# Kernel tuning notes

Hardware: AMD Instinct MI355X
Metric: run time of the kernel (lower is better)

Reference implementation:

```python
import jax, jax.numpy as jnp
import numpy as np

N = 256
IL_MMI = 0.02      # insertion loss MMI
IMB = 0.01         # imbalance MMI
IL_CR = 0.02       # insertion loss Crossing
CT = 0.01          # cross talk Crossing


def _mmi_matrix():
    # 2x2 MMI: sqrt(1-IL)*[[t, i r],[i r, t]] with t=sqrt((1+imb)/2), r=sqrt((1-imb)/2)
    a = np.sqrt(1.0 - IL_MMI)
    t = np.sqrt((1.0 + IMB) / 2.0)
    r = np.sqrt((1.0 - IMB) / 2.0)
    mmi2 = a * np.array([[t, 1j * r], [1j * r, t]], dtype=np.complex64)
    # block-diagonal over even pairs (0,1),(2,3),...
    return jnp.asarray(np.kron(np.eye(N // 2, dtype=np.complex64), mmi2))


def _crossing_matrix():
    # pairs start at odd index 1; rows 0 and N-1 pass through with amplitude sqrt(1-IL)*sqrt(1-CT)
    a = np.sqrt(1.0 - IL_CR)
    thru = a * np.sqrt(1.0 - CT)
    cr2 = a * np.array([[np.sqrt(CT), 1j * np.sqrt(1.0 - CT)],
                        [1j * np.sqrt(1.0 - CT), np.sqrt(CT)]], dtype=np.complex64)
    M = np.zeros((N, N), dtype=np.complex64)
    M[0, 0] = thru
    for i in range(1, N - 1, 2):
        M[i:i + 2, i:i + 2] = cr2
    if N % 2 == 0:
        M[-1, -1] = thru
    return jnp.asarray(M)


def setup_inputs() -> dict:
    key = jax.random.key(0)
    thetas = jax.random.uniform(key, (N // 2 + 2, N), dtype=jnp.float32) * (2.0 * np.pi)
    return {"thetas": thetas}


def reference(thetas):
    MMI = _mmi_matrix()
    CR = _crossing_matrix()
    phases = jnp.exp(1j * thetas)  # [N//2+2, N] complex64; diag phase-shift layers

    # arch = ht[0] @ I  (diagonal left-multiply == row scaling)
    arch0 = jnp.diag(phases[0])

    def body(arch, ph):
        # one mesh stage with trailing crossing (iterations i = 0 .. N//2-2)
        arch = MMI @ arch
        arch = ph[:, None] * arch      # ht[i+1] @ arch
        arch = MMI @ arch
        arch = CR @ arch
        return arch, None

    arch, _ = jax.lax.scan(body, arch0, phases[1:N // 2])

    # last loop iteration (i = N//2-1): no crossing
    arch = MMI @ arch
    arch = phases[N // 2][:, None] * arch
    arch = MMI @ arch
    # final phase layer ht[N//2+1]
    arch = phases[N // 2 + 1][:, None] * arch
    return arch
```

## Files before the change

kernel.cpp:

```cpp
#include <hip/hip_runtime.h>


constexpr int N = 256;

__global__ __launch_bounds__(64)
void neuropuls_chain_kernel(const float* __restrict__ thetas,
                            float2* __restrict__ Abuf,
                            float2* __restrict__ Bbuf)
{
    const int lane = threadIdx.x;
    const bool isB = blockIdx.x >= 256;
    const int col  = blockIdx.x & 255;

    const float AT = sqrtf(0.98f * 0.505f);
    const float AR = sqrtf(0.98f * 0.495f);
    const float BT = sqrtf(0.98f * 0.01f);
    const float BR = sqrtf(0.98f * 0.99f);

    float vr[4] = {0.f, 0.f, 0.f, 0.f};
    float vi[4] = {0.f, 0.f, 0.f, 0.f};

    {
        const int r0 = col - 4 * lane;
        if (0 <= r0 && r0 < 4) {
            if (isB) { vr[r0] = 1.f; vi[r0] = 0.f; }
            else {
                float s0, c0;
                __sincosf(thetas[col], &s0, &c0);
                vr[r0] = c0; vi[r0] = s0;
            }
        }
    }

    const int s0     = isB ? 65 : 1;
    const int nCross = isB ? 63 : 64;

    const float* tp = thetas + s0 * N + 4 * lane;

    auto mmi_pair = [&](int x, int y) {
        float xr = vr[x], xi = vi[x], yr = vr[y], yi = vi[y];
        vr[x] = AT * xr - AR * yi;  vi[x] = AT * xi + AR * yr;
        vr[y] = AT * yr - AR * xi;  vi[y] = AT * yi + AR * xr;
    };
    auto phase4c = [&](const float sn[4], const float cs[4]) {
        #pragma unroll
        for (int j = 0; j < 4; ++j) {
            float r = vr[j], i = vi[j];
            vr[j] = cs[j] * r - sn[j] * i;
            vi[j] = cs[j] * i + sn[j] * r;
        }
    };
    auto crossing = [&]() {
        float pv3r = __shfl_up(vr[3], 1);
        float pv3i = __shfl_up(vi[3], 1);
        float nv0r = __shfl_down(vr[0], 1);
        float nv0i = __shfl_down(vi[0], 1);
        {
            float xr = vr[1], xi = vi[1], yr = vr[2], yi = vi[2];
            vr[1] = BT * xr - BR * yi;  vi[1] = BT * xi + BR * yr;
            vr[2] = BT * yr - BR * xi;  vi[2] = BT * yi + BR * xr;
        }
        {
            float yr = vr[0], yi = vi[0];
            float nr = BT * yr - BR * pv3i;
            float ni = BT * yi + BR * pv3r;
            vr[0] = (lane == 0) ? BR * yr : nr;
            vi[0] = (lane == 0) ? BR * yi : ni;
        }
        {
            float xr = vr[3], xi = vi[3];
            float nr = BT * xr - BR * nv0i;
            float ni = BT * xi + BR * nv0r;
            vr[3] = (lane == 63) ? BR * xr : nr;
            vi[3] = (lane == 63) ? BR * xi : ni;
        }
    };
    auto sincos4 = [](float4 th, float sn[4], float cs[4]) {
        __sincosf(th.x, &sn[0], &cs[0]);
        __sincosf(th.y, &sn[1], &cs[1]);
        __sincosf(th.z, &sn[2], &cs[2]);
        __sincosf(th.w, &sn[3], &cs[3]);
    };

    float snA[4], csA[4];
    float4 thN;
    {
        float4 t1 = *(const float4*)tp;  tp += N;
        thN = *(const float4*)tp;        tp += N;
        sincos4(t1, snA, csA);
    }

    #pragma unroll 2
    for (int it = 0; it < nCross - 1; ++it) {
        float4 thNN = *(const float4*)tp;  tp += N;
        float snB[4], csB[4];
        sincos4(thN, snB, csB);
        mmi_pair(0, 1); mmi_pair(2, 3);
        phase4c(snA, csA);
        mmi_pair(0, 1); mmi_pair(2, 3);
        crossing();
        #pragma unroll
        for (int j = 0; j < 4; ++j) { snA[j] = snB[j]; csA[j] = csB[j]; }
        thN = thNN;
    }

    mmi_pair(0, 1); mmi_pair(2, 3);
    phase4c(snA, csA);
    mmi_pair(0, 1); mmi_pair(2, 3);
    crossing();

    if (isB) {
        float sn[4], cs[4];
        sincos4(thN, sn, cs);
        mmi_pair(0, 1); mmi_pair(2, 3);
        phase4c(sn, cs);
        mmi_pair(0, 1); mmi_pair(2, 3);
        float4 thF = *(const float4*)(thetas + 129 * N + 4 * lane);
        sincos4(thF, sn, cs);
        phase4c(sn, cs);
    }

    float2* dst = (isB ? Bbuf : Abuf) + col * N + 4 * lane;
    #pragma unroll
    for (int j = 0; j < 4; ++j) dst[j] = make_float2(vr[j], vi[j]);
}

__global__ __launch_bounds__(256)
void neuropuls_combine_kernel(const float2* __restrict__ Abuf,
                              const float2* __restrict__ Bbuf,
                              float* __restrict__ out)
{
    __shared__ float2 Acol[N];
    const int c = blockIdx.x;
    const int r = threadIdx.x;

    Acol[r] = Abuf[c * N + r];
    __syncthreads();

    float accr = 0.f, acci = 0.f;
    #pragma unroll 8
    for (int k = 0; k < N; ++k) {
        float2 b = Bbuf[k * N + r];
        float2 a = Acol[k];
        accr += b.x * a.x - b.y * a.y;
        acci += b.x * a.y + b.y * a.x;
    }

    out[r * N + c]         = accr;
    out[N * N + r * N + c] = acci;
}

extern "C" void kernel_launch(void* const* d_in, const int* in_sizes, int n_in,
                              void* d_out, int out_size, void* d_ws, size_t ws_size,
                              hipStream_t stream)
{
    const float* thetas = (const float*)d_in[0];
    float2* Abuf = (float2*)d_ws;
    float2* Bbuf = Abuf + N * N;
    float* out = (float*)d_out;
    (void)in_sizes; (void)n_in; (void)out_size; (void)ws_size;

    neuropuls_chain_kernel<<<dim3(512), dim3(64), 0, stream>>>(thetas, Abuf, Bbuf);
    neuropuls_combine_kernel<<<dim3(256), dim3(256), 0, stream>>>(Abuf, Bbuf, out);
}
```

Measured before the change: 85.43 us.

## Fuse MMI-phase-MMI into one 2x2 complex matrix and tile the combine GEMM

The chain kernel now folds the MMI, phase and MMI sequence into one precomputed 2x2 complex matrix per pair, built from sincos values. This cuts the FMAs on the serial critical path in each stage. The combine kernel becomes a shared-memory tiled complex GEMM with 32x32 output tiles and 2x2 register blocking per thread, replacing the per-column reduction that streamed all of B from global memory. It launches 64 blocks instead of 256, so fewer CUs are busy, but each loaded value is reused more.

Measured after the change: 100.3 us. 17.4% more time.

```diff
diff --git a/kernel.cpp b/kernel.cpp
--- a/kernel.cpp
+++ b/kernel.cpp
@@ -12,10 +12,11 @@
     const bool isB = blockIdx.x >= 256;
     const int col  = blockIdx.x & 255;
 
-    const float AT = sqrtf(0.98f * 0.505f);
-    const float AR = sqrtf(0.98f * 0.495f);
-    const float BT = sqrtf(0.98f * 0.01f);
-    const float BR = sqrtf(0.98f * 0.99f);
+    const float BT  = sqrtf(0.98f * 0.01f);
+    const float BR  = sqrtf(0.98f * 0.99f);
+    const float AT2 = 0.98f * 0.505f;
+    const float AR2 = 0.98f * 0.495f;
+    const float ATR = 0.98f * sqrtf(0.505f * 0.495f);
 
     float vr[4] = {0.f, 0.f, 0.f, 0.f};
     float vi[4] = {0.f, 0.f, 0.f, 0.f};
@@ -23,7 +24,7 @@
     {
         const int r0 = col - 4 * lane;
         if (0 <= r0 && r0 < 4) {
-            if (isB) { vr[r0] = 1.f; vi[r0] = 0.f; }
+            if (isB) { vr[r0] = 1.f; }
             else {
                 float s0, c0;
                 __sincosf(thetas[col], &s0, &c0);
@@ -34,20 +35,36 @@
 
     const int s0     = isB ? 65 : 1;
     const int nCross = isB ? 63 : 64;
-
     const float* tp = thetas + s0 * N + 4 * lane;
 
-    auto mmi_pair = [&](int x, int y) {
-        float xr = vr[x], xi = vi[x], yr = vr[y], yi = vi[y];
-        vr[x] = AT * xr - AR * yi;  vi[x] = AT * xi + AR * yr;
-        vr[y] = AT * yr - AR * xi;  vi[y] = AT * yi + AR * xr;
+    float F[2][6], G[2][6];
+
+    auto buildF = [&](float4 th, float Fd[2][6]) {
+        float sn[4], cs[4];
+        __sincosf(th.x, &sn[0], &cs[0]);
+        __sincosf(th.y, &sn[1], &cs[1]);
+        __sincosf(th.z, &sn[2], &cs[2]);
+        __sincosf(th.w, &sn[3], &cs[3]);
+        #pragma unroll
+        for (int j = 0; j < 2; ++j) {
+            const int x = 2 * j, y = 2 * j + 1;
+            Fd[j][0] = AT2 * cs[x] - AR2 * cs[y];
+            Fd[j][1] = AT2 * sn[x] - AR2 * sn[y];
+            Fd[j][2] = -ATR * (sn[x] + sn[y]);
+            Fd[j][3] =  ATR * (cs[x] + cs[y]);
+            Fd[j][4] = AT2 * cs[y] - AR2 * cs[x];
+            Fd[j][5] = AT2 * sn[y] - AR2 * sn[x];
+        }
     };
-    auto phase4c = [&](const float sn[4], const float cs[4]) {
-        #pragma unroll
-        for (int j = 0; j < 4; ++j) {
-            float r = vr[j], i = vi[j];
-            vr[j] = cs[j] * r - sn[j] * i;
-            vi[j] = cs[j] * i + sn[j] * r;
+    auto applyF = [&](const float Fd[2][6]) {
+        #pragma unroll
+        for (int j = 0; j < 2; ++j) {
+            const int x = 2 * j, y = 2 * j + 1;
+            float z0r = vr[x], z0i = vi[x], z1r = vr[y], z1i = vi[y];
+            vr[x] = Fd[j][0]*z0r - Fd[j][1]*z0i + Fd[j][2]*z1r - Fd[j][3]*z1i;
+            vi[x] = Fd[j][0]*z0i + Fd[j][1]*z0r + Fd[j][2]*z1i + Fd[j][3]*z1r;
+            vr[y] = Fd[j][2]*z0r - Fd[j][3]*z0i + Fd[j][4]*z1r - Fd[j][5]*z1i;
+            vi[y] = Fd[j][2]*z0i + Fd[j][3]*z0r + Fd[j][4]*z1i + Fd[j][5]*z1r;
         }
     };
     auto crossing = [&]() {
@@ -75,49 +92,43 @@
             vi[3] = (lane == 63) ? BR * xi : ni;
         }
     };
-    auto sincos4 = [](float4 th, float sn[4], float cs[4]) {
-        __sincosf(th.x, &sn[0], &cs[0]);
-        __sincosf(th.y, &sn[1], &cs[1]);
-        __sincosf(th.z, &sn[2], &cs[2]);
-        __sincosf(th.w, &sn[3], &cs[3]);
-    };
-
-    float snA[4], csA[4];
+
     float4 thN;
     {
         float4 t1 = *(const float4*)tp;  tp += N;
         thN = *(const float4*)tp;        tp += N;
-        sincos4(t1, snA, csA);
+        buildF(t1, F);
     }
 
     #pragma unroll 2
     for (int it = 0; it < nCross - 1; ++it) {
         float4 thNN = *(const float4*)tp;  tp += N;
-        float snB[4], csB[4];
-        sincos4(thN, snB, csB);
-        mmi_pair(0, 1); mmi_pair(2, 3);
-        phase4c(snA, csA);
-        mmi_pair(0, 1); mmi_pair(2, 3);
+        buildF(thN, G);
+        applyF(F);
         crossing();
         #pragma unroll
-        for (int j = 0; j < 4; ++j) { snA[j] = snB[j]; csA[j] = csB[j]; }
+        for (int j = 0; j < 2; ++j)
+            #pragma unroll
+            for (int q = 0; q < 6; ++q) F[j][q] = G[j][q];
         thN = thNN;
     }
 
-    mmi_pair(0, 1); mmi_pair(2, 3);
-    phase4c(snA, csA);
-    mmi_pair(0, 1); mmi_pair(2, 3);
+    applyF(F);
     crossing();
 
     if (isB) {
-        float sn[4], cs[4];
-        sincos4(thN, sn, cs);
-        mmi_pair(0, 1); mmi_pair(2, 3);
-        phase4c(sn, cs);
-        mmi_pair(0, 1); mmi_pair(2, 3);
+        buildF(thN, F);
+        applyF(F);
         float4 thF = *(const float4*)(thetas + 129 * N + 4 * lane);
-        sincos4(thF, sn, cs);
-        phase4c(sn, cs);
+        const float a[4] = {thF.x, thF.y, thF.z, thF.w};
+        #pragma unroll
+        for (int j = 0; j < 4; ++j) {
+            float sn, cs;
+            __sincosf(a[j], &sn, &cs);
+            float r = vr[j], i = vi[j];
+            vr[j] = cs * r - sn * i;
+            vi[j] = cs * i + sn * r;
+        }
     }
 
     float2* dst = (isB ? Bbuf : Abuf) + col * N + 4 * lane;
@@ -130,24 +141,58 @@
                               const float2* __restrict__ Bbuf,
                               float* __restrict__ out)
 {
-    __shared__ float2 Acol[N];
-    const int c = blockIdx.x;
-    const int r = threadIdx.x;
-
-    Acol[r] = Abuf[c * N + r];
-    __syncthreads();
-
-    float accr = 0.f, acci = 0.f;
-    #pragma unroll 8
-    for (int k = 0; k < N; ++k) {
-        float2 b = Bbuf[k * N + r];
-        float2 a = Acol[k];
-        accr += b.x * a.x - b.y * a.y;
-        acci += b.x * a.y + b.y * a.x;
-    }
-
-    out[r * N + c]         = accr;
-    out[N * N + r * N + c] = acci;
+    constexpr int PITCH = 34;
+    constexpr int TK    = 64;
+    __shared__ float2 Al[TK * PITCH];
+    __shared__ float2 Bl[TK * PITCH];
+
+    const int t   = threadIdx.x;
+    const int c0  = (blockIdx.x & 7) * 32;
+    const int r0  = (blockIdx.x >> 3) * 32;
+    const int cl2 = t & 15;
+    const int rq2 = t >> 4;
+
+    float ar00 = 0.f, ai00 = 0.f, ar01 = 0.f, ai01 = 0.f;
+    float ar10 = 0.f, ai10 = 0.f, ar11 = 0.f, ai11 = 0.f;
+
+    for (int kc = 0; kc < N; kc += TK) {
+        #pragma unroll
+        for (int j = 0; j < 4; ++j) {
+            int fl = t + j * 256;
+            int cl = fl >> 5;
+            int k4 = fl & 31;
+            float4 v = ((const float4*)(Abuf + (size_t)(c0 + cl) * N + kc))[k4];
+            Al[(2 * k4    ) * PITCH + cl] = make_float2(v.x, v.y);
+            Al[(2 * k4 + 1) * PITCH + cl] = make_float2(v.z, v.w);
+        }
+        #pragma unroll
+        for (int j = 0; j < 4; ++j) {
+            int fl  = t + j * 256;
+            int k   = fl >> 4;
+            int rl4 = fl & 15;
+            float4 v = ((const float4*)(Bbuf + (size_t)(kc + k) * N + r0))[rl4];
+            Bl[k * PITCH + 2 * rl4]     = make_float2(v.x, v.y);
+            Bl[k * PITCH + 2 * rl4 + 1] = make_float2(v.z, v.w);
+        }
+        __syncthreads();
+
+        #pragma unroll 4
+        for (int k = 0; k < TK; ++k) {
+            float4 a = *(const float4*)&Al[k * PITCH + 2 * cl2];
+            float4 b = *(const float4*)&Bl[k * PITCH + 2 * rq2];
+            ar00 += b.x * a.x - b.y * a.y;  ai00 += b.x * a.y + b.y * a.x;
+            ar01 += b.x * a.z - b.y * a.w;  ai01 += b.x * a.w + b.y * a.z;
+            ar10 += b.z * a.x - b.w * a.y;  ai10 += b.z * a.y + b.w * a.x;
+            ar11 += b.z * a.z - b.w * a.w;  ai11 += b.z * a.w + b.w * a.z;
+        }
+        __syncthreads();
+    }
+
+    const int r = r0 + 2 * rq2, c = c0 + 2 * cl2;
+    out[r * N + c]                 = ar00;  out[N * N + r * N + c]           = ai00;
+    out[r * N + c + 1]             = ar01;  out[N * N + r * N + c + 1]       = ai01;
+    out[(r + 1) * N + c]           = ar10;  out[N * N + (r + 1) * N + c]     = ai10;
+    out[(r + 1) * N + c + 1]       = ar11;  out[N * N + (r + 1) * N + c + 1] = ai11;
 }
 
 extern "C" void kernel_launch(void* const* d_in, const int* in_sizes, int n_in,
@@ -161,5 +206,5 @@
     (void)in_sizes; (void)n_in; (void)out_size; (void)ws_size;
 
     neuropuls_chain_kernel<<<dim3(512), dim3(64), 0, stream>>>(thetas, Abuf, Bbuf);
-    neuropuls_combine_kernel<<<dim3(256), dim3(256), 0, stream>>>(Abuf, Bbuf, out);
+    neuropuls_combine_kernel<<<dim3(64), dim3(256), 0, stream>>>(Abuf, Bbuf, out);
 }
```
